# Kernel optimization log

Measured on AMD Instinct MI355X. Metric: run time of the kernel, lower is better.

## Reference

```python
import jax, jax.numpy as jnp
import numpy as np

B, NX, NC, D, H = 2, 512, 4096, 1024, 16
HD = D // H  # head_dim = context_dim // heads
LN_EPS = 1e-5


def setup_inputs() -> dict:
    key = jax.random.key(0)
    k0, k1, k2, k3, k4 = jax.random.split(key, 5)
    x = jax.random.normal(k0, (B, NX, D), dtype=jnp.float32)
    c = jax.random.normal(k1, (B, NC, D), dtype=jnp.float32)
    attn_mask = jax.random.randint(k2, (B, NX, NC), 0, 2).astype(bool)
    # learned params
    ln_w = jnp.ones((D,), jnp.float32)
    ln_b = jnp.zeros((D,), jnp.float32)
    Wq = jax.random.normal(k3, (D, D), dtype=jnp.float32) * 0.02  # to_q (query_dim -> inner_dim)
    Wo = jax.random.normal(k4, (D, D), dtype=jnp.float32) * 0.02  # to_out (inner_dim -> query_dim)
    return {"x": x, "c": c, "attn_mask": attn_mask, "ln_w": ln_w, "ln_b": ln_b, "Wq": Wq, "Wo": Wo}


def _layernorm(x, w, b):
    mu = jnp.mean(x, axis=-1, keepdims=True)
    var = jnp.mean(jnp.square(x - mu), axis=-1, keepdims=True)
    return (x - mu) * jax.lax.rsqrt(var + LN_EPS) * w + b


def reference(x, c, attn_mask, ln_w, ln_b, Wq, Wo):
    scale = HD ** (-0.5)
    xn = _layernorm(x, ln_w, ln_b)
    q = (xn @ Wq).reshape(B, NX, H, HD).transpose(0, 2, 1, 3)      # (B,H,NX,HD)
    kv0 = c.reshape(B, NC, H, HD).transpose(0, 2, 1, 3)             # (B,H,NC,HD) -- kvt=(kv0,kv0)
    kv = jnp.concatenate([q, kv0], axis=2)                          # kv_append_q=True -> (B,H,NX+NC,HD)
    # mask: ones for the appended-q block, user mask for context block
    m = jnp.broadcast_to(attn_mask[:, None, :, :], (B, H, NX, NC))
    full_mask = jnp.concatenate([jnp.ones((B, H, NX, NX), bool), m], axis=-1)
    sim = jnp.einsum('bhqd,bhkd->bhqk', q * scale, kv)              # (B,H,NX,NX+NC)
    neg = -jnp.finfo(sim.dtype).max
    sim = jnp.where(full_mask, sim, neg)
    attn = jax.nn.softmax(sim, axis=-1)
    a = jnp.einsum('bhqk,bhkd->bhqd', attn, kv)
    o = a.transpose(0, 2, 1, 3).reshape(B, NX, H * HD) @ Wo
    return (o, kv0)
```

## Files before the change

kernel.cpp:

```cpp
#include <hip/hip_runtime.h>

#define B_  2
#define NX_ 512
#define NC_ 4096
#define D_  1024
#define H_  16
#define HD_ 64
#define NT_ (NX_ + NC_)
#define NSPLIT 4
#define KBS (NT_ / 64 / NSPLIT)

typedef float  floatx4  __attribute__((ext_vector_type(4)));
typedef __bf16 bf16x8   __attribute__((ext_vector_type(8)));
typedef unsigned short ushort8v __attribute__((ext_vector_type(8)));

__device__ __forceinline__ bf16x8 as_bf16x8(ushort8v u) {
    union { ushort8v u; bf16x8 b; } c; c.u = u; return c.b;
}
__device__ __forceinline__ unsigned short f2bf(float f) {
    unsigned u = __float_as_uint(f);
    u += 0x7FFF + ((u >> 16) & 1);
    return (unsigned short)(u >> 16);
}

__global__ __launch_bounds__(256)
void prep_kernel(const float* __restrict__ x, const float* __restrict__ lw,
                 const float* __restrict__ lb, const float* __restrict__ Wq,
                 const float* __restrict__ Wo, const int* __restrict__ mask,
                 const float* __restrict__ c,
                 unsigned short* __restrict__ xnb, unsigned short* __restrict__ WqT,
                 unsigned short* __restrict__ WoT, unsigned* __restrict__ bits,
                 unsigned short* __restrict__ cbf, float* __restrict__ gz,
                 float* __restrict__ kv0o) {
    int blk = blockIdx.x;
    int tid = threadIdx.x;
    if (blk < 1024) {
        int row = blk;
        float4 v = reinterpret_cast<const float4*>(x)[(size_t)row * (D_ / 4) + tid];
        float s  = v.x + v.y + v.z + v.w;
        float s2 = v.x * v.x + v.y * v.y + v.z * v.z + v.w * v.w;
        #pragma unroll
        for (int off = 32; off > 0; off >>= 1) {
            s  += __shfl_down(s, off);
            s2 += __shfl_down(s2, off);
        }
        __shared__ float sm[4], sm2[4], stat[2];
        int wv = tid >> 6;
        if ((tid & 63) == 0) { sm[wv] = s; sm2[wv] = s2; }
        __syncthreads();
        if (tid == 0) {
            float S  = sm[0] + sm[1] + sm[2] + sm[3];
            float S2 = sm2[0] + sm2[1] + sm2[2] + sm2[3];
            float mu  = S * (1.0f / D_);
            float var = fmaxf(S2 * (1.0f / D_) - mu * mu, 0.0f);
            stat[0] = mu;
            stat[1] = rsqrtf(var + 1e-5f);
        }
        __syncthreads();
        float mu = stat[0], rs = stat[1];
        float4 w4 = reinterpret_cast<const float4*>(lw)[tid];
        float4 b4 = reinterpret_cast<const float4*>(lb)[tid];
        ushort4 o;
        o.x = f2bf((v.x - mu) * rs * w4.x + b4.x);
        o.y = f2bf((v.y - mu) * rs * w4.y + b4.y);
        o.z = f2bf((v.z - mu) * rs * w4.z + b4.z);
        o.w = f2bf((v.w - mu) * rs * w4.w + b4.w);
        reinterpret_cast<ushort4*>(xnb)[(size_t)row * (D_ / 4) + tid] = o;
    } else if (blk < 1536) {
        int which = (blk - 1024) >> 8;
        int t = (blk - 1024) & 255;
        const float* W = which ? Wo : Wq;
        unsigned short* WT = which ? WoT : WqT;
        __shared__ unsigned short T[64][72];
        int row0 = (t >> 4) * 64, col0 = (t & 15) * 64;
        int r = tid >> 2, ch = (tid & 3) * 16;
        const float* src = W + (size_t)(row0 + r) * D_ + col0 + ch;
        unsigned short vals[16];
        #pragma unroll
        for (int k = 0; k < 4; ++k) {
            float4 v = reinterpret_cast<const float4*>(src)[k];
            vals[k*4+0] = f2bf(v.x); vals[k*4+1] = f2bf(v.y);
            vals[k*4+2] = f2bf(v.z); vals[k*4+3] = f2bf(v.w);
        }
        #pragma unroll
        for (int i = 0; i < 16; ++i) T[ch + i][r] = vals[i];
        __syncthreads();
        unsigned short* dst = WT + (size_t)(col0 + r) * D_ + row0 + ch;
        uint4 o0 = *reinterpret_cast<uint4*>(&T[r][ch]);
        uint4 o1 = *reinterpret_cast<uint4*>(&T[r][ch + 8]);
        *reinterpret_cast<uint4*>(dst)     = o0;
        *reinterpret_cast<uint4*>(dst + 8) = o1;
    } else if (blk < 2048) {
        size_t w = (size_t)(blk - 1536) * 256 + tid;
        const int* src = mask + w * 32;
        unsigned b = 0;
        #pragma unroll
        for (int k = 0; k < 8; ++k) {
            int4 v = reinterpret_cast<const int4*>(src)[k];
            b |= (v.x != 0 ? 1u : 0u) << (k * 4 + 0);
            b |= (v.y != 0 ? 1u : 0u) << (k * 4 + 1);
            b |= (v.z != 0 ? 1u : 0u) << (k * 4 + 2);
            b |= (v.w != 0 ? 1u : 0u) << (k * 4 + 3);
        }
        bits[w] = b;
    } else if (blk < 10240) {
        size_t i = ((size_t)(blk - 2048) * 256 + tid) * 4;
        float4 v = *reinterpret_cast<const float4*>(c + i);
        ushort4 o;
        o.x = f2bf(v.x); o.y = f2bf(v.y); o.z = f2bf(v.z); o.w = f2bf(v.w);
        *reinterpret_cast<ushort4*>(cbf + i) = o;
        if (kv0o != nullptr) {
            size_t row = i >> 10;
            int dd = (int)(i & 1023);
            int hh = dd >> 6, d4 = (dd & 63) >> 2;
            int bb = (int)(row >> 12);
            int n  = (int)(row & 4095);
            size_t o4 = (((size_t)(bb * 16 + hh) * NC_ + n) << 4) + d4;
            reinterpret_cast<float4*>(kv0o)[o4] = v;
        }
    } else {
        size_t i = ((size_t)(blk - 10240) * 256 + tid) * 4;
        float4 z = {0.f, 0.f, 0.f, 0.f};
        *reinterpret_cast<float4*>(gz + i) = z;
    }
}

__global__ __launch_bounds__(256)
void kv0_kernel(const float* __restrict__ c, float* __restrict__ out2) {
    size_t i = (size_t)blockIdx.x * 256 + threadIdx.x;
    int d4 = (int)(i & 15);
    size_t r = i >> 4;
    int n = (int)(r % NC_);
    size_t r2 = r / NC_;
    int h = (int)(r2 & (H_ - 1));
    int b = (int)(r2 >> 4);
    float4 v = *reinterpret_cast<const float4*>(c + ((size_t)(b * NC_ + n)) * D_ + h * HD_ + d4 * 4);
    reinterpret_cast<float4*>(out2)[i] = v;
}

__global__ __launch_bounds__(256)
void gemm_bt_kernel(const unsigned short* __restrict__ A, const unsigned short* __restrict__ BT,
                    unsigned short* __restrict__ Cb) {
    __shared__ unsigned short As[64][72];
    __shared__ unsigned short Bs[64][72];
    int tid = threadIdx.x;
    int lane = tid & 63, wave = tid >> 6;
    int m16 = lane & 15, g = lane >> 4, g8 = g * 8;
    int row0 = blockIdx.y * 64, col0 = blockIdx.x * 64;
    int r = tid >> 2, ch = (tid & 3) * 16;

    floatx4 acc[4];
    #pragma unroll
    for (int t = 0; t < 4; ++t) acc[t] = (floatx4){0.f, 0.f, 0.f, 0.f};

    const unsigned short* abase = A  + (size_t)(row0 + r) * D_ + ch;
    const unsigned short* bbase = BT + (size_t)(col0 + r) * D_ + ch;
    uint4 a0 = *reinterpret_cast<const uint4*>(abase);
    uint4 a1 = *reinterpret_cast<const uint4*>(abase + 8);
    uint4 b0 = *reinterpret_cast<const uint4*>(bbase);
    uint4 b1 = *reinterpret_cast<const uint4*>(bbase + 8);

    for (int kc = 0; kc < 16; ++kc) {
        if (kc) {
            asm volatile("s_waitcnt lgkmcnt(0)" ::: "memory");
            __builtin_amdgcn_s_barrier();
        }
        *reinterpret_cast<uint4*>(&As[r][ch])     = a0;
        *reinterpret_cast<uint4*>(&As[r][ch + 8]) = a1;
        *reinterpret_cast<uint4*>(&Bs[r][ch])     = b0;
        *reinterpret_cast<uint4*>(&Bs[r][ch + 8]) = b1;
        if (kc < 15) {
            int k0 = (kc + 1) * 64;
            a0 = *reinterpret_cast<const uint4*>(abase + k0);
            a1 = *reinterpret_cast<const uint4*>(abase + k0 + 8);
            b0 = *reinterpret_cast<const uint4*>(bbase + k0);
            b1 = *reinterpret_cast<const uint4*>(bbase + k0 + 8);
        }
        asm volatile("s_waitcnt lgkmcnt(0)" ::: "memory");
        __builtin_amdgcn_s_barrier();
        bf16x8 fa0 = as_bf16x8(*reinterpret_cast<ushort8v*>(&As[16 * wave + m16][g8]));
        bf16x8 fa1 = as_bf16x8(*reinterpret_cast<ushort8v*>(&As[16 * wave + m16][32 + g8]));
        #pragma unroll
        for (int t = 0; t < 4; ++t) {
            bf16x8 fb0 = as_bf16x8(*reinterpret_cast<ushort8v*>(&Bs[16 * t + m16][g8]));
            bf16x8 fb1 = as_bf16x8(*reinterpret_cast<ushort8v*>(&Bs[16 * t + m16][32 + g8]));
            acc[t] = __builtin_amdgcn_mfma_f32_16x16x32_bf16(fa0, fb0, acc[t], 0, 0, 0);
            acc[t] = __builtin_amdgcn_mfma_f32_16x16x32_bf16(fa1, fb1, acc[t], 0, 0, 0);
        }
    }
    #pragma unroll
    for (int t = 0; t < 4; ++t)
        #pragma unroll
        for (int reg = 0; reg < 4; ++reg)
            Cb[(size_t)(row0 + 16 * wave + g * 4 + reg) * D_ + col0 + 16 * t + m16] = f2bf(acc[t][reg]);
}

__global__ __launch_bounds__(256)
void gemm_attn_kernel(const float* __restrict__ gacc, const float* __restrict__ gacc_l,
                      const unsigned short* __restrict__ BT, float* __restrict__ out) {
    __shared__ unsigned short As[64][72];
    __shared__ unsigned short Bs[64][72];
    int tid = threadIdx.x;
    int lane = tid & 63, wave = tid >> 6;
    int m16 = lane & 15, g = lane >> 4, g8 = g * 8;
    int row0 = blockIdx.y * 64, col0 = blockIdx.x * 64;
    int r = tid >> 2, ch = (tid & 3) * 16;
    int row = row0 + r;

    floatx4 acc[4];
    #pragma unroll
    for (int t = 0; t < 4; ++t) acc[t] = (floatx4){0.f, 0.f, 0.f, 0.f};

    const float* abase = gacc + (size_t)row * D_ + ch;
    const unsigned short* bbase = BT + (size_t)(col0 + r) * D_ + ch;
    float4 av4[4];
    uint4 b0, b1;
    float inv = 1.0f / fmaxf(gacc_l[(size_t)row * H_ + 0], 1e-35f);
    #pragma unroll
    for (int t = 0; t < 4; ++t) av4[t] = reinterpret_cast<const float4*>(abase)[t];
    b0 = *reinterpret_cast<const uint4*>(bbase);
    b1 = *reinterpret_cast<const uint4*>(bbase + 8);

    for (int kc = 0; kc < 16; ++kc) {
        if (kc) {
            asm volatile("s_waitcnt lgkmcnt(0)" ::: "memory");
            __builtin_amdgcn_s_barrier();
        }
        unsigned short av[16];
        #pragma unroll
        for (int t = 0; t < 4; ++t) {
            av[t*4+0] = f2bf(av4[t].x * inv); av[t*4+1] = f2bf(av4[t].y * inv);
            av[t*4+2] = f2bf(av4[t].z * inv); av[t*4+3] = f2bf(av4[t].w * inv);
        }
        *reinterpret_cast<uint4*>(&As[r][ch])     = *reinterpret_cast<uint4*>(&av[0]);
        *reinterpret_cast<uint4*>(&As[r][ch + 8]) = *reinterpret_cast<uint4*>(&av[8]);
        *reinterpret_cast<uint4*>(&Bs[r][ch])     = b0;
        *reinterpret_cast<uint4*>(&Bs[r][ch + 8]) = b1;
        if (kc < 15) {
            int k0 = (kc + 1) * 64;
            inv = 1.0f / fmaxf(gacc_l[(size_t)row * H_ + kc + 1], 1e-35f);
            #pragma unroll
            for (int t = 0; t < 4; ++t) av4[t] = reinterpret_cast<const float4*>(abase + k0)[t];
            b0 = *reinterpret_cast<const uint4*>(bbase + k0);
            b1 = *reinterpret_cast<const uint4*>(bbase + k0 + 8);
        }
        asm volatile("s_waitcnt lgkmcnt(0)" ::: "memory");
        __builtin_amdgcn_s_barrier();
        bf16x8 fa0 = as_bf16x8(*reinterpret_cast<ushort8v*>(&As[16 * wave + m16][g8]));
        bf16x8 fa1 = as_bf16x8(*reinterpret_cast<ushort8v*>(&As[16 * wave + m16][32 + g8]));
        #pragma unroll
        for (int t = 0; t < 4; ++t) {
            bf16x8 fb0 = as_bf16x8(*reinterpret_cast<ushort8v*>(&Bs[16 * t + m16][g8]));
            bf16x8 fb1 = as_bf16x8(*reinterpret_cast<ushort8v*>(&Bs[16 * t + m16][32 + g8]));
            acc[t] = __builtin_amdgcn_mfma_f32_16x16x32_bf16(fa0, fb0, acc[t], 0, 0, 0);
            acc[t] = __builtin_amdgcn_mfma_f32_16x16x32_bf16(fa1, fb1, acc[t], 0, 0, 0);
        }
    }
    #pragma unroll
    for (int t = 0; t < 4; ++t)
        #pragma unroll
        for (int reg = 0; reg < 4; ++reg)
            out[(size_t)(row0 + 16 * wave + g * 4 + reg) * D_ + col0 + 16 * t + m16] = acc[t][reg];
}

__global__ __launch_bounds__(256, 4)
void attn_kernel(const unsigned short* __restrict__ qbf,
                 const unsigned short* __restrict__ cbf,
                 const unsigned* __restrict__ maskbits,
                 float* __restrict__ gacc, float* __restrict__ gacc_l) {
    int blk   = blockIdx.x;
    int bh    = ((blk >> 8) << 3) | (blk & 7);
    int inner = (blk >> 3) & 31;
    int qt    = inner & 7;
    int split = inner >> 3;
    int h  = bh & 15;
    int b  = bh >> 4;
    int tid  = threadIdx.x;
    int lane = tid & 63;
    int wave = tid >> 6;
    int m16  = lane & 15;
    int g    = lane >> 4;
    int g8   = g * 8;

    __shared__ unsigned short Ks [64][72];
    __shared__ unsigned short Kts[64][72];
    __shared__ unsigned short Ps [64][64];

    const unsigned short* qrow = qbf + ((size_t)(b * NX_ + qt * 64 + 16 * wave + m16)) * D_ + h * HD_;
    bf16x8 qa0 = as_bf16x8(*reinterpret_cast<const ushort8v*>(qrow + g8));
    bf16x8 qa1 = as_bf16x8(*reinterpret_cast<const ushort8v*>(qrow + 32 + g8));

    floatx4 acc_o[4];
    #pragma unroll
    for (int td = 0; td < 4; ++td) acc_o[td] = (floatx4){0.f, 0.f, 0.f, 0.f};
    floatx4 acc_l = (floatx4){0.f, 0.f, 0.f, 0.f};

    ushort8v ones_u;
    #pragma unroll
    for (int j = 0; j < 8; ++j) ones_u[j] = 0x3F80;
    bf16x8 onesf = as_bf16x8(ones_u);

    int Kg = tid >> 4;
    int Dg = tid & 15;
    int pcst = ((Kg >> 1) + (Dg >> 1)) & 7;
    int prsw = 2 * ((m16 >> 2) & 3);

    int kb0 = split * KBS;

    uint2 rows[4];
    {
        const unsigned short* s0 = (kb0 < 8)
            ? qbf + ((size_t)(b * NX_ + kb0 * 64 + 4 * Kg)) * D_ + h * HD_ + 4 * Dg
            : cbf + ((size_t)(b * NC_ + kb0 * 64 - NX_ + 4 * Kg)) * D_ + h * HD_ + 4 * Dg;
        #pragma unroll
        for (int kk = 0; kk < 4; ++kk)
            rows[kk] = *reinterpret_cast<const uint2*>(s0 + (size_t)kk * D_);
    }

    for (int i = 0; i < KBS; ++i) {
        int kb = kb0 + i;
        asm volatile("s_waitcnt lgkmcnt(0)" ::: "memory");
        __builtin_amdgcn_s_barrier();

        unsigned mw0[4], mw1[4];
        if (kb >= 8) {
            #pragma unroll
            for (int r = 0; r < 4; ++r) {
                size_t mi = ((size_t)(b * NX_ + qt * 64 + 16 * wave + g * 4 + r)) * (NC_ / 32)
                          + (size_t)(kb - 8) * 2;
                uint2 w = *reinterpret_cast<const uint2*>(&maskbits[mi]);
                mw0[r] = w.x; mw1[r] = w.y;
            }
        }

        #pragma unroll
        for (int kk = 0; kk < 4; ++kk)
            *reinterpret_cast<uint2*>(&Ks[4 * Kg + kk][4 * Dg]) = rows[kk];
        #pragma unroll
        for (int i2 = 0; i2 < 4; ++i2) {
            unsigned sel = (i2 & 1) ? 0x07060302u : 0x05040100u;
            unsigned r0 = (i2 >> 1) ? rows[0].y : rows[0].x;
            unsigned r1 = (i2 >> 1) ? rows[1].y : rows[1].x;
            unsigned r2 = (i2 >> 1) ? rows[2].y : rows[2].x;
            unsigned r3 = (i2 >> 1) ? rows[3].y : rows[3].x;
            uint2 cw;
            cw.x = __builtin_amdgcn_perm(r1, r0, sel);
            cw.y = __builtin_amdgcn_perm(r3, r2, sel);
            *reinterpret_cast<uint2*>(&Kts[4 * Dg + i2][pcst * 8 + 4 * (Kg & 1)]) = cw;
        }

        {
            int kbn = (i + 1 < KBS) ? kb + 1 : kb;
            const unsigned short* sn = (kbn < 8)
                ? qbf + ((size_t)(b * NX_ + kbn * 64 + 4 * Kg)) * D_ + h * HD_ + 4 * Dg
                : cbf + ((size_t)(b * NC_ + kbn * 64 - NX_ + 4 * Kg)) * D_ + h * HD_ + 4 * Dg;
            #pragma unroll
            for (int kk = 0; kk < 4; ++kk)
                rows[kk] = *reinterpret_cast<const uint2*>(sn + (size_t)kk * D_);
        }

        asm volatile("s_waitcnt lgkmcnt(0)" ::: "memory");
        __builtin_amdgcn_s_barrier();
        __builtin_amdgcn_sched_barrier(0);
        asm volatile("" ::: "memory");

        floatx4 accs[4];
        __builtin_amdgcn_s_setprio(1);
        #pragma unroll
        for (int t = 0; t < 4; ++t) {
            bf16x8 b0 = as_bf16x8(*reinterpret_cast<ushort8v*>(&Ks[16 * t + m16][g8]));
            bf16x8 b1 = as_bf16x8(*reinterpret_cast<ushort8v*>(&Ks[16 * t + m16][32 + g8]));
            floatx4 d = (floatx4){0.f, 0.f, 0.f, 0.f};
            d = __builtin_amdgcn_mfma_f32_16x16x32_bf16(qa0, b0, d, 0, 0, 0);
            d = __builtin_amdgcn_mfma_f32_16x16x32_bf16(qa1, b1, d, 0, 0, 0);
            accs[t] = d;
        }
        __builtin_amdgcn_s_setprio(0);

        const float C1 = 0.18033688011112042f;
        const float C2 = 92.33248261689366f;
        #pragma unroll
        for (int t = 0; t < 4; ++t) {
            int cc = 2 * t + (m16 >> 3);
            #pragma unroll
            for (int r = 0; r < 4; ++r) {
                float e = fminf(fmaf(accs[t][r], C1, -C2), 0.0f);
                float p = __builtin_amdgcn_exp2f(e);
                if (kb >= 8) {
                    unsigned w = (t < 2) ? mw0[r] : mw1[r];
                    unsigned bit = (w >> ((16 * t + m16) & 31)) & 1u;
                    p = bit ? p : 0.0f;
                }
                int prow = 16 * wave + g * 4 + r;
                int pc = (cc + 2 * g) & 7;
                Ps[prow][pc * 8 + (m16 & 7)] = (unsigned short)(__float_as_uint(p) >> 16);
            }
        }
        asm volatile("s_waitcnt lgkmcnt(0)" ::: "memory");

        bf16x8 p0 = as_bf16x8(*reinterpret_cast<ushort8v*>(&Ps[16 * wave + m16][((g + prsw) & 7) * 8]));
        bf16x8 p1 = as_bf16x8(*reinterpret_cast<ushort8v*>(&Ps[16 * wave + m16][((4 + g + prsw) & 7) * 8]));
        __builtin_amdgcn_s_setprio(1);
        acc_l = __builtin_amdgcn_mfma_f32_16x16x32_bf16(p0, onesf, acc_l, 0, 0, 0);
        acc_l = __builtin_amdgcn_mfma_f32_16x16x32_bf16(p1, onesf, acc_l, 0, 0, 0);
        #pragma unroll
        for (int td = 0; td < 4; ++td) {
            int row = 16 * td + m16;
            int rh = row >> 3;
            bf16x8 v0 = as_bf16x8(*reinterpret_cast<ushort8v*>(&Kts[row][((g + rh) & 7) * 8]));
            bf16x8 v1 = as_bf16x8(*reinterpret_cast<ushort8v*>(&Kts[row][((4 + g + rh) & 7) * 8]));
            acc_o[td] = __builtin_amdgcn_mfma_f32_16x16x32_bf16(p0, v0, acc_o[td], 0, 0, 0);
            acc_o[td] = __builtin_amdgcn_mfma_f32_16x16x32_bf16(p1, v1, acc_o[td], 0, 0, 0);
        }
        __builtin_amdgcn_s_setprio(0);
    }

    #pragma unroll
    for (int r = 0; r < 4; ++r) {
        int qrow_ = qt * 64 + 16 * wave + g * 4 + r;
        float* dst = gacc + ((size_t)(b * NX_ + qrow_)) * D_ + h * HD_;
        #pragma unroll
        for (int td = 0; td < 4; ++td)
            unsafeAtomicAdd(&dst[16 * td + m16], acc_o[td][r]);
        if (m16 == 0)
            unsafeAtomicAdd(&gacc_l[(size_t)(b * NX_ + qrow_) * H_ + h], acc_l[r]);
    }
}

extern "C" void kernel_launch(void* const* d_in, const int* in_sizes, int n_in,
                              void* d_out, int out_size, void* d_ws, size_t ws_size,
                              hipStream_t stream) {
    (void)in_sizes; (void)n_in; (void)out_size;
    const float* x    = (const float*)d_in[0];
    const float* c    = (const float*)d_in[1];
    const int*   mask = (const int*)d_in[2];
    const float* ln_w = (const float*)d_in[3];
    const float* ln_b = (const float*)d_in[4];
    const float* Wq   = (const float*)d_in[5];
    const float* Wo   = (const float*)d_in[6];
    float* out  = (float*)d_out;
    float* out2 = out + (size_t)B_ * NX_ * D_;

    const size_t SCRATCH_FLOATS = 8011776;
    bool use_ws = (d_ws != nullptr) && (ws_size >= SCRATCH_FLOATS * sizeof(float));
    float* base = use_ws ? (float*)d_ws : out2;

    unsigned short* qbf      = (unsigned short*)(base);
    unsigned*       maskbits = (unsigned*)(base + 524288);
    float*          gacc     = base + 655360;
    float*          gacc_l   = base + 1703936;
    unsigned short* WqT      = (unsigned short*)(base + 1720320);
    unsigned short* WoT      = (unsigned short*)(base + 2244608);
    unsigned short* xnb      = (unsigned short*)(base + 2768896);
    unsigned short* cbf      = (unsigned short*)(base + 3817472);

    prep_kernel<<<11280, 256, 0, stream>>>(x, ln_w, ln_b, Wq, Wo, mask, c,
                                           xnb, WqT, WoT, maskbits, cbf, gacc,
                                           use_ws ? out2 : nullptr);
    gemm_bt_kernel<<<dim3(16, 16), 256, 0, stream>>>(xnb, WqT, qbf);
    attn_kernel<<<NSPLIT * 256, 256, 0, stream>>>(qbf, cbf, maskbits, gacc, gacc_l);
    gemm_attn_kernel<<<dim3(16, 16), 256, 0, stream>>>(gacc, gacc_l, WoT, out);
    if (!use_ws)
        kv0_kernel<<<(B_ * H_ * NC_ * HD_ / 4) / 256, 256, 0, stream>>>(c, out2);
}
```

Before: 182.5 us.

## Process two query tiles per block to reuse staged K/V, double split count

Each attention block now handles 128 query rows (two 64-row subtiles) against the same staged K/V tile in shared memory, and the key dimension is split 8 ways instead of 4, so the grid stays at 1024 blocks. Each K/V tile load and transpose into LDS is shared by twice as many queries, halving global K/V traffic and staging work per unit of compute. The cost is doubled accumulator registers (two acc_o sets), a larger P buffer in LDS, and twice as many atomic adds to the global accumulator because there are more key splits. The s_setprio hints were also dropped.

Result: slower. 211.0 us (+15.6%).

```diff
diff --git a/kernel.cpp b/kernel.cpp
--- a/kernel.cpp
+++ b/kernel.cpp
@@ -7,7 +7,7 @@
 #define H_  16
 #define HD_ 64
 #define NT_ (NX_ + NC_)
-#define NSPLIT 4
+#define NSPLIT 8
 #define KBS (NT_ / 64 / NSPLIT)
 
 typedef float  floatx4  __attribute__((ext_vector_type(4)));
@@ -271,8 +271,8 @@
     int blk   = blockIdx.x;
     int bh    = ((blk >> 8) << 3) | (blk & 7);
     int inner = (blk >> 3) & 31;
-    int qt    = inner & 7;
-    int split = inner >> 3;
+    int qt2   = inner & 3;
+    int split = inner >> 2;
     int h  = bh & 15;
     int b  = bh >> 4;
     int tid  = threadIdx.x;
@@ -284,16 +284,25 @@
 
     __shared__ unsigned short Ks [64][72];
     __shared__ unsigned short Kts[64][72];
-    __shared__ unsigned short Ps [64][64];
-
-    const unsigned short* qrow = qbf + ((size_t)(b * NX_ + qt * 64 + 16 * wave + m16)) * D_ + h * HD_;
-    bf16x8 qa0 = as_bf16x8(*reinterpret_cast<const ushort8v*>(qrow + g8));
-    bf16x8 qa1 = as_bf16x8(*reinterpret_cast<const ushort8v*>(qrow + 32 + g8));
-
-    floatx4 acc_o[4];
-    #pragma unroll
-    for (int td = 0; td < 4; ++td) acc_o[td] = (floatx4){0.f, 0.f, 0.f, 0.f};
-    floatx4 acc_l = (floatx4){0.f, 0.f, 0.f, 0.f};
+    __shared__ unsigned short Ps [128][64];
+
+    bf16x8 qa[2][2];
+    #pragma unroll
+    for (int s = 0; s < 2; ++s) {
+        const unsigned short* qrow = qbf
+            + ((size_t)(b * NX_ + qt2 * 128 + s * 64 + 16 * wave + m16)) * D_ + h * HD_;
+        qa[s][0] = as_bf16x8(*reinterpret_cast<const ushort8v*>(qrow + g8));
+        qa[s][1] = as_bf16x8(*reinterpret_cast<const ushort8v*>(qrow + 32 + g8));
+    }
+
+    floatx4 acc_o[2][4];
+    floatx4 acc_l[2];
+    #pragma unroll
+    for (int s = 0; s < 2; ++s) {
+        #pragma unroll
+        for (int td = 0; td < 4; ++td) acc_o[s][td] = (floatx4){0.f, 0.f, 0.f, 0.f};
+        acc_l[s] = (floatx4){0.f, 0.f, 0.f, 0.f};
+    }
 
     ushort8v ones_u;
     #pragma unroll
@@ -322,15 +331,17 @@
         asm volatile("s_waitcnt lgkmcnt(0)" ::: "memory");
         __builtin_amdgcn_s_barrier();
 
-        unsigned mw0[4], mw1[4];
+        unsigned mw0[2][4], mw1[2][4];
         if (kb >= 8) {
             #pragma unroll
-            for (int r = 0; r < 4; ++r) {
-                size_t mi = ((size_t)(b * NX_ + qt * 64 + 16 * wave + g * 4 + r)) * (NC_ / 32)
-                          + (size_t)(kb - 8) * 2;
-                uint2 w = *reinterpret_cast<const uint2*>(&maskbits[mi]);
-                mw0[r] = w.x; mw1[r] = w.y;
-            }
+            for (int s = 0; s < 2; ++s)
+                #pragma unroll
+                for (int r = 0; r < 4; ++r) {
+                    size_t mi = ((size_t)(b * NX_ + qt2 * 128 + s * 64 + 16 * wave + g * 4 + r))
+                                * (NC_ / 32) + (size_t)(kb - 8) * 2;
+                    uint2 w = *reinterpret_cast<const uint2*>(&maskbits[mi]);
+                    mw0[s][r] = w.x; mw1[s][r] = w.y;
+                }
         }
 
         #pragma unroll
@@ -364,67 +375,71 @@
         __builtin_amdgcn_sched_barrier(0);
         asm volatile("" ::: "memory");
 
-        floatx4 accs[4];
-        __builtin_amdgcn_s_setprio(1);
-        #pragma unroll
-        for (int t = 0; t < 4; ++t) {
-            bf16x8 b0 = as_bf16x8(*reinterpret_cast<ushort8v*>(&Ks[16 * t + m16][g8]));
-            bf16x8 b1 = as_bf16x8(*reinterpret_cast<ushort8v*>(&Ks[16 * t + m16][32 + g8]));
-            floatx4 d = (floatx4){0.f, 0.f, 0.f, 0.f};
-            d = __builtin_amdgcn_mfma_f32_16x16x32_bf16(qa0, b0, d, 0, 0, 0);
-            d = __builtin_amdgcn_mfma_f32_16x16x32_bf16(qa1, b1, d, 0, 0, 0);
-            accs[t] = d;
-        }
-        __builtin_amdgcn_s_setprio(0);
-
         const float C1 = 0.18033688011112042f;
         const float C2 = 92.33248261689366f;
-        #pragma unroll
-        for (int t = 0; t < 4; ++t) {
-            int cc = 2 * t + (m16 >> 3);
-            #pragma unroll
-            for (int r = 0; r < 4; ++r) {
-                float e = fminf(fmaf(accs[t][r], C1, -C2), 0.0f);
-                float p = __builtin_amdgcn_exp2f(e);
-                if (kb >= 8) {
-                    unsigned w = (t < 2) ? mw0[r] : mw1[r];
-                    unsigned bit = (w >> ((16 * t + m16) & 31)) & 1u;
-                    p = bit ? p : 0.0f;
+
+        #pragma unroll
+        for (int s = 0; s < 2; ++s) {
+            floatx4 accs[4];
+            #pragma unroll
+            for (int t = 0; t < 4; ++t) {
+                bf16x8 b0 = as_bf16x8(*reinterpret_cast<ushort8v*>(&Ks[16 * t + m16][g8]));
+                bf16x8 b1 = as_bf16x8(*reinterpret_cast<ushort8v*>(&Ks[16 * t + m16][32 + g8]));
+                floatx4 d = (floatx4){0.f, 0.f, 0.f, 0.f};
+                d = __builtin_amdgcn_mfma_f32_16x16x32_bf16(qa[s][0], b0, d, 0, 0, 0);
+                d = __builtin_amdgcn_mfma_f32_16x16x32_bf16(qa[s][1], b1, d, 0, 0, 0);
+                accs[t] = d;
+            }
+
+            #pragma unroll
+            for (int t = 0; t < 4; ++t) {
+                int cc = 2 * t + (m16 >> 3);
+                #pragma unroll
+                for (int r = 0; r < 4; ++r) {
+                    float e = fminf(fmaf(accs[t][r], C1, -C2), 0.0f);
+                    float p = __builtin_amdgcn_exp2f(e);
+                    if (kb >= 8) {
+                        unsigned w = (t < 2) ? mw0[s][r] : mw1[s][r];
+                        unsigned bit = (w >> ((16 * t + m16) & 31)) & 1u;
+                        p = bit ? p : 0.0f;
+                    }
+                    int prow = 64 * s + 16 * wave + g * 4 + r;
+                    int pc = (cc + 2 * g) & 7;
+                    Ps[prow][pc * 8 + (m16 & 7)] = (unsigned short)(__float_as_uint(p) >> 16);
                 }
-                int prow = 16 * wave + g * 4 + r;
-                int pc = (cc + 2 * g) & 7;
-                Ps[prow][pc * 8 + (m16 & 7)] = (unsigned short)(__float_as_uint(p) >> 16);
             }
-        }
-        asm volatile("s_waitcnt lgkmcnt(0)" ::: "memory");
-
-        bf16x8 p0 = as_bf16x8(*reinterpret_cast<ushort8v*>(&Ps[16 * wave + m16][((g + prsw) & 7) * 8]));
-        bf16x8 p1 = as_bf16x8(*reinterpret_cast<ushort8v*>(&Ps[16 * wave + m16][((4 + g + prsw) & 7) * 8]));
-        __builtin_amdgcn_s_setprio(1);
-        acc_l = __builtin_amdgcn_mfma_f32_16x16x32_bf16(p0, onesf, acc_l, 0, 0, 0);
-        acc_l = __builtin_amdgcn_mfma_f32_16x16x32_bf16(p1, onesf, acc_l, 0, 0, 0);
-        #pragma unroll
-        for (int td = 0; td < 4; ++td) {
-            int row = 16 * td + m16;
-            int rh = row >> 3;
-            bf16x8 v0 = as_bf16x8(*reinterpret_cast<ushort8v*>(&Kts[row][((g + rh) & 7) * 8]));
-            bf16x8 v1 = as_bf16x8(*reinterpret_cast<ushort8v*>(&Kts[row][((4 + g + rh) & 7) * 8]));
-            acc_o[td] = __builtin_amdgcn_mfma_f32_16x16x32_bf16(p0, v0, acc_o[td], 0, 0, 0);
-            acc_o[td] = __builtin_amdgcn_mfma_f32_16x16x32_bf16(p1, v1, acc_o[td], 0, 0, 0);
-        }
-        __builtin_amdgcn_s_setprio(0);
-    }
-
-    #pragma unroll
-    for (int r = 0; r < 4; ++r) {
-        int qrow_ = qt * 64 + 16 * wave + g * 4 + r;
-        float* dst = gacc + ((size_t)(b * NX_ + qrow_)) * D_ + h * HD_;
-        #pragma unroll
-        for (int td = 0; td < 4; ++td)
-            unsafeAtomicAdd(&dst[16 * td + m16], acc_o[td][r]);
-        if (m16 == 0)
-            unsafeAtomicAdd(&gacc_l[(size_t)(b * NX_ + qrow_) * H_ + h], acc_l[r]);
-    }
+            asm volatile("s_waitcnt lgkmcnt(0)" ::: "memory");
+
+            bf16x8 p0 = as_bf16x8(*reinterpret_cast<ushort8v*>(
+                &Ps[64 * s + 16 * wave + m16][((g + prsw) & 7) * 8]));
+            bf16x8 p1 = as_bf16x8(*reinterpret_cast<ushort8v*>(
+                &Ps[64 * s + 16 * wave + m16][((4 + g + prsw) & 7) * 8]));
+            acc_l[s] = __builtin_amdgcn_mfma_f32_16x16x32_bf16(p0, onesf, acc_l[s], 0, 0, 0);
+            acc_l[s] = __builtin_amdgcn_mfma_f32_16x16x32_bf16(p1, onesf, acc_l[s], 0, 0, 0);
+            #pragma unroll
+            for (int td = 0; td < 4; ++td) {
+                int row = 16 * td + m16;
+                int rh = row >> 3;
+                bf16x8 v0 = as_bf16x8(*reinterpret_cast<ushort8v*>(&Kts[row][((g + rh) & 7) * 8]));
+                bf16x8 v1 = as_bf16x8(*reinterpret_cast<ushort8v*>(&Kts[row][((4 + g + rh) & 7) * 8]));
+                acc_o[s][td] = __builtin_amdgcn_mfma_f32_16x16x32_bf16(p0, v0, acc_o[s][td], 0, 0, 0);
+                acc_o[s][td] = __builtin_amdgcn_mfma_f32_16x16x32_bf16(p1, v1, acc_o[s][td], 0, 0, 0);
+            }
+        }
+    }
+
+    #pragma unroll
+    for (int s = 0; s < 2; ++s)
+        #pragma unroll
+        for (int r = 0; r < 4; ++r) {
+            int qrow_ = qt2 * 128 + s * 64 + 16 * wave + g * 4 + r;
+            float* dst = gacc + ((size_t)(b * NX_ + qrow_)) * D_ + h * HD_;
+            #pragma unroll
+            for (int td = 0; td < 4; ++td)
+                unsafeAtomicAdd(&dst[16 * td + m16], acc_o[s][td][r]);
+            if (m16 == 0)
+                unsafeAtomicAdd(&gacc_l[(size_t)(b * NX_ + qrow_) * H_ + h], acc_l[s][r]);
+        }
 }
 
 extern "C" void kernel_launch(void* const* d_in, const int* in_sizes, int n_in,
@@ -458,7 +473,7 @@
                                            xnb, WqT, WoT, maskbits, cbf, gacc,
                                            use_ws ? out2 : nullptr);
     gemm_bt_kernel<<<dim3(16, 16), 256, 0, stream>>>(xnb, WqT, qbf);
-    attn_kernel<<<NSPLIT * 256, 256, 0, stream>>>(qbf, cbf, maskbits, gacc, gacc_l);
+    attn_kernel<<<1024, 256, 0, stream>>>(qbf, cbf, maskbits, gacc, gacc_l);
     gemm_attn_kernel<<<dim3(16, 16), 256, 0, stream>>>(gacc, gacc_l, WoT, out);
     if (!use_ws)
         kv0_kernel<<<(B_ * H_ * NC_ * HD_ / 4) / 256, 256, 0, stream>>>(c, out2);
```
